# Kernel tuning notes

Hardware: AMD Instinct MI355X
Metric: run time of the kernel (lower is better)

## Reference

```python
import jax, jax.numpy as jnp
import numpy as np

INV_SQRT2 = 0.7071067811865476
SCALES = 3


def dwt_analysis(x, dec_lo, dec_hi, scales):
    """Multi-level 1D DWT along last axis (pywt/ptwt convention).
    x: [B, D]. dec_lo/dec_hi are cross-correlation filters (torch conv1d
    semantics, i.e. the flipped pywt decomposition filters as stored by the
    repo). Returns [cA_s | cD_s | ... | cD_1] truncated to the last D columns
    (identity for Haar on power-of-two D)."""
    flen = dec_lo.shape[0]
    pad = (2 * flen - 3) // 2  # ptwt zero-pad; 0 for Haar (flen=2)
    filt = jnp.stack([dec_lo, dec_hi])[:, None, :]  # [2, 1, flen]
    lo = x[:, None, :]  # [B, 1, D]
    highs = []
    for _ in range(scales):
        out = jax.lax.conv_general_dilated(
            lo, filt, window_strides=(2,), padding=[(pad, pad)],
            dimension_numbers=('NCH', 'OIH', 'NCH'))  # [B, 2, D/2]
        lo = out[:, 0:1, :]
        highs.append(out[:, 1, :])
    coeffs = jnp.concatenate([lo[:, 0, :]] + highs[::-1], axis=-1)
    return coeffs[:, -x.shape[-1]:]


def setup_inputs() -> dict:
    key = jax.random.key(0)
    k1, k2, k3, k4, k5 = jax.random.split(key, 5)
    B, D = 4096, 4096
    x = jax.random.normal(k1, (B, D), jnp.float32)
    diag_s = jax.random.normal(k2, (D,), jnp.float32)
    diag_g = jax.random.normal(k3, (D,), jnp.float32)
    diag_b = jax.random.normal(k4, (D,), jnp.float32)
    perm = jax.random.permutation(k5, jnp.arange(D))  # random column permutation
    # Haar analysis filters in cross-correlation (torch conv1d) orientation
    dec_lo = jnp.array([INV_SQRT2, INV_SQRT2], jnp.float32)
    dec_hi = jnp.array([INV_SQRT2, -INV_SQRT2], jnp.float32)
    return {"x": x, "diag_s": diag_s, "diag_g": diag_g, "diag_b": diag_b,
            "dec_lo": dec_lo, "dec_hi": dec_hi, "perm": perm, "scales": SCALES}


def reference(x, diag_s, diag_g, diag_b, dec_lo, dec_hi, perm, scales):
    # mul_b: x @ diag(b) == columnwise scale (same math, no O(d^2) matmul)
    h = x * diag_b
    h = dwt_analysis(h, dec_lo, dec_hi, scales)
    # mul_p: x @ P for a permutation matrix == column gather
    h = jnp.take(h, perm, axis=1)
    h = h * diag_g  # mul_g
    h = dwt_analysis(h, dec_lo, dec_hi, scales)
    return h * diag_s  # mul_s
```

## Files before the change

kernel.cpp:

```cpp
#include <hip/hip_runtime.h>


#define D   4096
#define NT  256

#define C_INV_SQRT2 0.70710678118654752440f

typedef float vf2 __attribute__((ext_vector_type(2)));
typedef float vf4 __attribute__((ext_vector_type(4)));

static __device__ __forceinline__ void haar_chunk(
    float v0, float v1, float v2, float v3, int odd,
    float& d1a, float& d1b, float& d2v, float& l3)
{
    float a10 = (v0 + v1) * C_INV_SQRT2;
    d1a       = (v0 - v1) * C_INV_SQRT2;
    float a11 = (v2 + v3) * C_INV_SQRT2;
    d1b       = (v2 - v3) * C_INV_SQRT2;
    float a2  = (a10 + a11) * C_INV_SQRT2;
    d2v       = (a10 - a11) * C_INV_SQRT2;
    float a2p = __shfl_xor(a2, 1);
    l3 = (odd ? (a2p - a2) : (a2 + a2p)) * C_INV_SQRT2;
}

__global__ __launch_bounds__(NT, 8) void wavelet_rows_kernel(
    const float* __restrict__ x,
    const float* __restrict__ diag_s,
    const float* __restrict__ diag_g,
    const float* __restrict__ diag_b,
    const int*   __restrict__ perm,
    float*       __restrict__ out)
{
    __shared__ float buf[D];

    const int t   = threadIdx.x;
    const int s   = t >> 1;
    const int odd = t & 1;
    const size_t row = (size_t)blockIdx.x;

    const vf4*  b4 = (const vf4*)diag_b;
    const vf4*  g4 = (const vf4*)diag_g;
    const int4* p4 = (const int4*)perm;
    const vf2*  s2 = (const vf2*)diag_s;

    const vf4* x4 = (const vf4*)(x + row * (size_t)D);
    #pragma unroll
    for (int k = 0; k < 4; ++k) {
        vf4 xv = x4[256 * k + t];
        vf4 bv = b4[256 * k + t];
        float d1a, d1b, d2v, l3;
        haar_chunk(xv.x * bv.x, xv.y * bv.y,
                   xv.z * bv.z, xv.w * bv.w, odd,
                   d1a, d1b, d2v, l3);
        vf2 dp; dp.x = d1a; dp.y = d1b;
        *(vf2*)&buf[2048 + 512 * k + 2 * t] = dp;
        buf[1024 + 256 * k + t] = d2v;
        buf[(odd ? 512 : 0) + 128 * k + s] = l3;
    }

    int4 pidx[4];
    #pragma unroll
    for (int k = 0; k < 4; ++k) pidx[k] = p4[256 * k + t];

    __syncthreads();

    float* orow = out + row * (size_t)D;
    #pragma unroll
    for (int k = 0; k < 4; ++k) {
        vf4  gv  = g4[256 * k + t];
        vf2  s1  = s2[1024 + 256 * k + t];
        float sv2 = diag_s[1024 + 256 * k + t];
        float sv3 = diag_s[(odd ? 512 : 0) + 128 * k + s];

        float w0 = buf[pidx[k].x] * gv.x;
        float w1 = buf[pidx[k].y] * gv.y;
        float w2 = buf[pidx[k].z] * gv.z;
        float w3 = buf[pidx[k].w] * gv.w;
        float e1a, e1b, e2v, f3;
        haar_chunk(w0, w1, w2, w3, odd, e1a, e1b, e2v, f3);

        vf2 ep; ep.x = e1a * s1.x; ep.y = e1b * s1.y;
        __builtin_nontemporal_store(ep, &((vf2*)orow)[1024 + 256 * k + t]);
        __builtin_nontemporal_store(e2v * sv2, &orow[1024 + 256 * k + t]);
        __builtin_nontemporal_store(f3 * sv3,
                                    &orow[(odd ? 512 : 0) + 128 * k + s]);
    }
}

extern "C" void kernel_launch(void* const* d_in, const int* in_sizes, int n_in,
                              void* d_out, int out_size, void* d_ws, size_t ws_size,
                              hipStream_t stream) {
    const float* x      = (const float*)d_in[0];
    const float* diag_s = (const float*)d_in[1];
    const float* diag_g = (const float*)d_in[2];
    const float* diag_b = (const float*)d_in[3];
    const int* perm     = (const int*)d_in[6];
    float* out          = (float*)d_out;

    wavelet_rows_kernel<<<4096, NT, 0, stream>>>(x, diag_s, diag_g, diag_b, perm, out);
}
```

Measured before the change: 126.5 us.

## Use single-wavefront blocks processing two rows each without barriers

Shrinks each block to one 64-thread wavefront that handles two rows in turn, looping 16 chunks per row instead of 4. The intent is to drop the __syncthreads between the two wavelet stages, since a single wave executes its LDS writes and reads in order, and to cut the block count in half. The trade-off is that each 16KB LDS buffer now supports only one wave, so fewer waves fit per CU to hide memory latency. Permutation indices are also reloaded per row instead of held in registers.

```diff
diff --git a/kernel.cpp b/kernel.cpp
--- a/kernel.cpp
+++ b/kernel.cpp
@@ -2,7 +2,8 @@
 
 
 #define D   4096
-#define NT  256
+#define NT  64
+#define R   2
 
 #define C_INV_SQRT2 0.70710678118654752440f
 
@@ -23,7 +24,7 @@
     l3 = (odd ? (a2p - a2) : (a2 + a2p)) * C_INV_SQRT2;
 }
 
-__global__ __launch_bounds__(NT, 8) void wavelet_rows_kernel(
+__global__ __launch_bounds__(NT) void wavelet_wave_kernel(
     const float* __restrict__ x,
     const float* __restrict__ diag_s,
     const float* __restrict__ diag_g,
@@ -34,56 +35,55 @@
     __shared__ float buf[D];
 
     const int t   = threadIdx.x;
-    const int s   = t >> 1;
+    const int s_  = t >> 1;
     const int odd = t & 1;
-    const size_t row = (size_t)blockIdx.x;
+    const size_t row0 = (size_t)blockIdx.x * R;
 
     const vf4*  b4 = (const vf4*)diag_b;
     const vf4*  g4 = (const vf4*)diag_g;
     const int4* p4 = (const int4*)perm;
     const vf2*  s2 = (const vf2*)diag_s;
 
-    const vf4* x4 = (const vf4*)(x + row * (size_t)D);
-    #pragma unroll
-    for (int k = 0; k < 4; ++k) {
-        vf4 xv = x4[256 * k + t];
-        vf4 bv = b4[256 * k + t];
-        float d1a, d1b, d2v, l3;
-        haar_chunk(xv.x * bv.x, xv.y * bv.y,
-                   xv.z * bv.z, xv.w * bv.w, odd,
-                   d1a, d1b, d2v, l3);
-        vf2 dp; dp.x = d1a; dp.y = d1b;
-        *(vf2*)&buf[2048 + 512 * k + 2 * t] = dp;
-        buf[1024 + 256 * k + t] = d2v;
-        buf[(odd ? 512 : 0) + 128 * k + s] = l3;
-    }
+    for (int r = 0; r < R; ++r) {
+        const vf4* x4 = (const vf4*)(x + (row0 + r) * (size_t)D);
 
-    int4 pidx[4];
-    #pragma unroll
-    for (int k = 0; k < 4; ++k) pidx[k] = p4[256 * k + t];
+        #pragma unroll
+        for (int k = 0; k < 16; ++k) {
+            vf4 xv = x4[64 * k + t];
+            vf4 bv = b4[64 * k + t];
+            float d1a, d1b, d2v, l3;
+            haar_chunk(xv.x * bv.x, xv.y * bv.y,
+                       xv.z * bv.z, xv.w * bv.w, odd,
+                       d1a, d1b, d2v, l3);
+            vf2 dp; dp.x = d1a; dp.y = d1b;
+            *(vf2*)&buf[2048 + 128 * k + 2 * t] = dp;
+            buf[1024 + 64 * k + t] = d2v;
+            buf[(odd ? 512 : 0) + 32 * k + s_] = l3;
+        }
 
-    __syncthreads();
 
-    float* orow = out + row * (size_t)D;
-    #pragma unroll
-    for (int k = 0; k < 4; ++k) {
-        vf4  gv  = g4[256 * k + t];
-        vf2  s1  = s2[1024 + 256 * k + t];
-        float sv2 = diag_s[1024 + 256 * k + t];
-        float sv3 = diag_s[(odd ? 512 : 0) + 128 * k + s];
+        float* orow = out + (row0 + r) * (size_t)D;
+        #pragma unroll
+        for (int k = 0; k < 16; ++k) {
+            int4  pv  = p4[64 * k + t];
+            vf4   gv  = g4[64 * k + t];
+            vf2   s1  = s2[1024 + 64 * k + t];
+            float sv2 = diag_s[1024 + 64 * k + t];
+            float sv3 = diag_s[(odd ? 512 : 0) + 32 * k + s_];
 
-        float w0 = buf[pidx[k].x] * gv.x;
-        float w1 = buf[pidx[k].y] * gv.y;
-        float w2 = buf[pidx[k].z] * gv.z;
-        float w3 = buf[pidx[k].w] * gv.w;
-        float e1a, e1b, e2v, f3;
-        haar_chunk(w0, w1, w2, w3, odd, e1a, e1b, e2v, f3);
+            float w0 = buf[pv.x] * gv.x;
+            float w1 = buf[pv.y] * gv.y;
+            float w2 = buf[pv.z] * gv.z;
+            float w3 = buf[pv.w] * gv.w;
+            float e1a, e1b, e2v, f3;
+            haar_chunk(w0, w1, w2, w3, odd, e1a, e1b, e2v, f3);
 
-        vf2 ep; ep.x = e1a * s1.x; ep.y = e1b * s1.y;
-        __builtin_nontemporal_store(ep, &((vf2*)orow)[1024 + 256 * k + t]);
-        __builtin_nontemporal_store(e2v * sv2, &orow[1024 + 256 * k + t]);
-        __builtin_nontemporal_store(f3 * sv3,
-                                    &orow[(odd ? 512 : 0) + 128 * k + s]);
+            vf2 ep; ep.x = e1a * s1.x; ep.y = e1b * s1.y;
+            __builtin_nontemporal_store(ep, &((vf2*)orow)[1024 + 64 * k + t]);
+            __builtin_nontemporal_store(e2v * sv2, &orow[1024 + 64 * k + t]);
+            __builtin_nontemporal_store(f3 * sv3,
+                                        &orow[(odd ? 512 : 0) + 32 * k + s_]);
+        }
     }
 }
 
@@ -97,5 +97,6 @@
     const int* perm     = (const int*)d_in[6];
     float* out          = (float*)d_out;
 
-    wavelet_rows_kernel<<<4096, NT, 0, stream>>>(x, diag_s, diag_g, diag_b, perm, out);
+    wavelet_wave_kernel<<<4096 / R, NT, 0, stream>>>(x, diag_s, diag_g, diag_b,
+                                                     perm, out);
 }
```

New measurement: 151.7 us. 1.2x slower.
